# Optimization experiments

Measured on AMD Instinct MI355X. Metric: run time of the kernel, lower is better.

Reference implementation:

```python
import jax, jax.numpy as jnp
import numpy as np

B, L, H = 4, 512, 768          # batch, seq_len, bert hidden
S, R = 100, 100                # num candidate spans, num relation pairs
E = 128                        # size embedding dim
TE, TR = 8, 6                  # entity / relation types
MAX_ENT_LEN = 100
NEG = -1e20


def _span_masks(rng, b, n, seq_len, max_len):
    # contiguous span masks with lengths in [1, max_len-1] so sum(-1) < max_len
    starts = rng.integers(0, seq_len - 1, size=(b, n))
    lengths = rng.integers(1, max_len, size=(b, n))
    ends = np.minimum(starts + lengths, seq_len)
    pos = np.arange(seq_len)
    m = (pos[None, None, :] >= starts[..., None]) & (pos[None, None, :] < ends[..., None])
    return jnp.asarray(m.astype(np.int32))


def setup_inputs() -> dict:
    rng = np.random.default_rng(0)
    key = jax.random.key(0)
    k = jax.random.split(key, 6)
    return {
        "last_hidden_state": jax.random.normal(k[0], (B, L, H), jnp.float32),
        "entity_mask": _span_masks(rng, B, S, L, MAX_ENT_LEN),
        "relations": jnp.asarray(rng.integers(0, S, size=(B, R, 2)).astype(np.int32)),
        "relation_context_mask": _span_masks(rng, B, R, L, MAX_ENT_LEN),
        "relation_sample_mask": jnp.asarray(rng.integers(0, 2, size=(B, R)).astype(np.int32)),
        "size_emb": jax.random.normal(k[1], (MAX_ENT_LEN, E), jnp.float32) * 0.02,
        "span_w": jax.random.normal(k[2], (E + 2 * H, TE), jnp.float32) * 0.02,
        "span_b": jnp.zeros((TE,), jnp.float32),
        "rel_w": jax.random.normal(k[3], (2 * E + 3 * H, TR), jnp.float32) * 0.02,
        "rel_b": jnp.zeros((TR,), jnp.float32),
    }


def _masked_max(h, mask):
    # h: [B,L,H], mask: [B,N,L] int {0,1} -> [B,N,H]
    mf = mask[..., None].astype(h.dtype)                       # [B,N,L,1]
    masked = jnp.where(mf == 0, jnp.asarray(NEG, h.dtype), h[:, None] * mf)
    return masked.max(axis=2)


def reference(last_hidden_state, entity_mask, relations, relation_context_mask,
              relation_sample_mask, size_emb, span_w, span_b, rel_w, rel_b):
    b = last_hidden_state.shape[0]
    # ---- entity classification ----
    context = last_hidden_state[:, 0]                          # CLS pooling [B,H]
    entity_size = size_emb[entity_mask.sum(-1)]                # [B,S,E]
    entity = _masked_max(last_hidden_state, entity_mask)       # [B,S,H]
    ctx = jnp.broadcast_to(context[:, None], (b, entity.shape[1], context.shape[-1]))
    entity_repr = jnp.concatenate([entity, ctx, entity_size], axis=-1)
    entity_logit = entity_repr @ span_w + span_b               # [B,S,TE]
    # ---- relation classification ----
    rel_ctx = _masked_max(last_hidden_state, relation_context_mask)  # [B,R,H]
    rel_ctx = jnp.where(relation_sample_mask[..., None] == 1,
                        jnp.zeros((), rel_ctx.dtype), rel_ctx)
    r = relations.shape[1]
    flat = relations.reshape(b, r * 2)                         # [B,2R]
    pair = jnp.take_along_axis(entity, flat[..., None], axis=1).reshape(b, r, -1)      # [B,R,2H]
    pair_size = jnp.take_along_axis(entity_size, flat[..., None], axis=1).reshape(b, r, -1)  # [B,R,2E]
    relation_repr = jnp.concatenate([rel_ctx, pair, pair_size], axis=-1)
    relation_logit = relation_repr @ rel_w + rel_b             # [B,R,TR]
    return entity_logit, relation_logit
```

## Files before the change

### kernel.cpp

```cpp
#include <hip/hip_runtime.h>

#define Bn 4
#define Ln 512
#define Hn 768
#define Sn 100
#define Rn 100
#define En 128
#define TEn 8
#define TRn 6
#define NEGF (-1e20f)
#define H4 (Hn / 4)
#define E4 (En / 4)

__device__ __forceinline__ float4 fmax4(float4 a, float4 b) {
    return make_float4(fmaxf(a.x, b.x), fmaxf(a.y, b.y),
                       fmaxf(a.z, b.z), fmaxf(a.w, b.w));
}

__global__ void __launch_bounds__(192)
span_kernel(const float* __restrict__ hid,
            const int* __restrict__ ent_mask,
            const int* __restrict__ rel_mask,
            const int* __restrict__ samp_mask,
            const float* __restrict__ size_emb,
            const float* __restrict__ span_w,
            const float* __restrict__ span_b,
            float* __restrict__ entity,
            float* __restrict__ relctx,
            int* __restrict__ entcnt,
            float* __restrict__ out_ent) {
    int blk = blockIdx.x;
    int tid = threadIdx.x;
    int lane = tid & 63;
    int b = blk / (Sn + Rn);
    int idx = blk % (Sn + Rn);
    bool is_rel = idx >= Sn;
    int span = is_rel ? idx - Sn : idx;

    float4* out4 = (float4*)(is_rel ? relctx + ((size_t)b * Rn + span) * Hn
                                    : entity + ((size_t)b * Sn + span) * Hn) + tid;

    bool zero_out = is_rel && (samp_mask[b * Rn + span] == 1);
    if (zero_out) {
        *out4 = make_float4(0.f, 0.f, 0.f, 0.f);
        return;
    }

    const int* mask = is_rel ? rel_mask + ((size_t)b * Rn + span) * Ln
                             : ent_mask + ((size_t)b * Sn + span) * Ln;
    const int4* m4 = (const int4*)(mask + lane * 8);
    int4 ma = m4[0], mb = m4[1];
    int mm[8] = {ma.x, ma.y, ma.z, ma.w, mb.x, mb.y, mb.z, mb.w};
    int cnt = 0, first = 0x7fffffff, last = -1;
    #pragma unroll
    for (int r = 0; r < 8; ++r) {
        if (mm[r] != 0) {
            int row = lane * 8 + r;
            ++cnt;
            first = min(first, row);
            last = max(last, row);
        }
    }
    #pragma unroll
    for (int off = 1; off < 64; off <<= 1) {
        cnt += __shfl_xor(cnt, off, 64);
        first = min(first, __shfl_xor(first, off, 64));
        last = max(last, __shfl_xor(last, off, 64));
    }
    int start = first, end = last + 1;

    const float4* hb4 = (const float4*)(hid + (size_t)b * Ln * Hn) + tid;
    float4 m = make_float4(NEGF, NEGF, NEGF, NEGF);
    int r = start;
    for (; r + 4 <= end; r += 4) {
        float4 v0 = hb4[(size_t)(r + 0) * H4];
        float4 v1 = hb4[(size_t)(r + 1) * H4];
        float4 v2 = hb4[(size_t)(r + 2) * H4];
        float4 v3 = hb4[(size_t)(r + 3) * H4];
        m = fmax4(m, fmax4(fmax4(v0, v1), fmax4(v2, v3)));
    }
    for (; r < end; ++r)
        m = fmax4(m, hb4[(size_t)r * H4]);

    *out4 = m;

    if (is_rel) return;
    if (tid == 0) entcnt[b * Sn + span] = cnt;

    float acc[TEn];
    #pragma unroll
    for (int t = 0; t < TEn; ++t) acc[t] = 0.0f;

    const float* vv = &m.x;
    #pragma unroll
    for (int j = 0; j < 4; ++j) {
        const float4* w4 = (const float4*)(span_w + (size_t)(4 * tid + j) * TEn);
        float4 wa = w4[0], wb = w4[1];
        acc[0] += vv[j] * wa.x; acc[1] += vv[j] * wa.y;
        acc[2] += vv[j] * wa.z; acc[3] += vv[j] * wa.w;
        acc[4] += vv[j] * wb.x; acc[5] += vv[j] * wb.y;
        acc[6] += vv[j] * wb.z; acc[7] += vv[j] * wb.w;
    }
    float4 c = ((const float4*)(hid + (size_t)b * Ln * Hn))[tid];
    const float* cc = &c.x;
    #pragma unroll
    for (int j = 0; j < 4; ++j) {
        const float4* w4 = (const float4*)(span_w + (size_t)(Hn + 4 * tid + j) * TEn);
        float4 wa = w4[0], wb = w4[1];
        acc[0] += cc[j] * wa.x; acc[1] += cc[j] * wa.y;
        acc[2] += cc[j] * wa.z; acc[3] += cc[j] * wa.w;
        acc[4] += cc[j] * wb.x; acc[5] += cc[j] * wb.y;
        acc[6] += cc[j] * wb.z; acc[7] += cc[j] * wb.w;
    }
    if (tid < E4) {
        float4 sv = ((const float4*)(size_emb + (size_t)cnt * En))[tid];
        const float* ss = &sv.x;
        #pragma unroll
        for (int j = 0; j < 4; ++j) {
            const float4* w4 = (const float4*)(span_w + (size_t)(2 * Hn + 4 * tid + j) * TEn);
            float4 wa = w4[0], wb = w4[1];
            acc[0] += ss[j] * wa.x; acc[1] += ss[j] * wa.y;
            acc[2] += ss[j] * wa.z; acc[3] += ss[j] * wa.w;
            acc[4] += ss[j] * wb.x; acc[5] += ss[j] * wb.y;
            acc[6] += ss[j] * wb.z; acc[7] += ss[j] * wb.w;
        }
    }

    #pragma unroll
    for (int t = 0; t < TEn; ++t)
        #pragma unroll
        for (int off = 32; off > 0; off >>= 1)
            acc[t] += __shfl_down(acc[t], off, 64);
    __shared__ float red[3][TEn];
    int wave = tid >> 6;
    if (lane == 0) {
        #pragma unroll
        for (int t = 0; t < TEn; ++t) red[wave][t] = acc[t];
    }
    __syncthreads();
    if (tid < TEn) {
        float s = span_b[tid];
        #pragma unroll
        for (int w = 0; w < 3; ++w) s += red[w][tid];
        out_ent[(size_t)(b * Sn + span) * TEn + tid] = s;
    }
}

__global__ void __launch_bounds__(256)
rel_logit_kernel(const float* __restrict__ entity,
                 const float* __restrict__ relctx,
                 const int* __restrict__ relations,
                 const int* __restrict__ entcnt,
                 const float* __restrict__ size_emb,
                 const float* __restrict__ rel_w,
                 const float* __restrict__ rel_b,
                 float* __restrict__ out_rel) {
    int blk = blockIdx.x;
    int b = blk / Rn;
    int tid = threadIdx.x;
    int a0 = relations[blk * 2 + 0];
    int a1 = relations[blk * 2 + 1];
    const float4* ctx4 = (const float4*)(relctx + (size_t)blk * Hn);
    const float4* e04  = (const float4*)(entity + ((size_t)b * Sn + a0) * Hn);
    const float4* e14  = (const float4*)(entity + ((size_t)b * Sn + a1) * Hn);
    const float4* s04  = (const float4*)(size_emb + (size_t)entcnt[b * Sn + a0] * En);
    const float4* s14  = (const float4*)(size_emb + (size_t)entcnt[b * Sn + a1] * En);

    float acc[TRn];
    #pragma unroll
    for (int t = 0; t < TRn; ++t) acc[t] = 0.0f;

    const int K4 = 3 * H4 + 2 * E4;
    for (int k4 = tid; k4 < K4; k4 += 256) {
        float4 v;
        if (k4 < H4)               v = ctx4[k4];
        else if (k4 < 2 * H4)      v = e04[k4 - H4];
        else if (k4 < 3 * H4)      v = e14[k4 - 2 * H4];
        else if (k4 < 3 * H4 + E4) v = s04[k4 - 3 * H4];
        else                       v = s14[k4 - 3 * H4 - E4];
        int k = k4 * 4;
        const float* vp = &v.x;
        #pragma unroll
        for (int j = 0; j < 4; ++j) {
            const float2* wr = (const float2*)(rel_w + (size_t)(k + j) * TRn);
            float2 w0 = wr[0], w1 = wr[1], w2 = wr[2];
            acc[0] += vp[j] * w0.x; acc[1] += vp[j] * w0.y;
            acc[2] += vp[j] * w1.x; acc[3] += vp[j] * w1.y;
            acc[4] += vp[j] * w2.x; acc[5] += vp[j] * w2.y;
        }
    }

    #pragma unroll
    for (int t = 0; t < TRn; ++t)
        #pragma unroll
        for (int off = 32; off > 0; off >>= 1)
            acc[t] += __shfl_down(acc[t], off, 64);
    __shared__ float red[4][TRn];
    int wave = tid >> 6, lane = tid & 63;
    if (lane == 0) {
        #pragma unroll
        for (int t = 0; t < TRn; ++t) red[wave][t] = acc[t];
    }
    __syncthreads();
    if (tid < TRn) {
        float s = rel_b[tid];
        #pragma unroll
        for (int w = 0; w < 4; ++w) s += red[w][tid];
        out_rel[(size_t)blk * TRn + tid] = s;
    }
}

extern "C" void kernel_launch(void* const* d_in, const int* in_sizes, int n_in,
                              void* d_out, int out_size, void* d_ws, size_t ws_size,
                              hipStream_t stream) {
    const float* hid       = (const float*)d_in[0];
    const int*   ent_mask  = (const int*)d_in[1];
    const int*   relations = (const int*)d_in[2];
    const int*   rel_mask  = (const int*)d_in[3];
    const int*   samp_mask = (const int*)d_in[4];
    const float* size_emb  = (const float*)d_in[5];
    const float* span_w    = (const float*)d_in[6];
    const float* span_b    = (const float*)d_in[7];
    const float* rel_w     = (const float*)d_in[8];
    const float* rel_b     = (const float*)d_in[9];

    float* out = (float*)d_out;
    float* out_ent = out;
    float* out_rel = out + Bn * Sn * TEn;

    char* ws = (char*)d_ws;
    float* entity = (float*)ws;
    float* relctx = entity + (size_t)Bn * Sn * Hn;
    int*   entcnt = (int*)(relctx + (size_t)Bn * Rn * Hn);

    span_kernel<<<Bn * (Sn + Rn), 192, 0, stream>>>(
        hid, ent_mask, rel_mask, samp_mask, size_emb, span_w, span_b,
        entity, relctx, entcnt, out_ent);

    rel_logit_kernel<<<Bn * Rn, 256, 0, stream>>>(
        entity, relctx, relations, entcnt, size_emb, rel_w, rel_b, out_rel);
}
```

Measured before the change: 26.22 us.

## Precompute 8-row block maxima and fuse span max with logits into one kernel

Adds a first kernel that reduces the hidden states into per-8-row block maxima. A single logits kernel then computes span maxima from these block maxima plus partial edge rows. The relation blocks recompute their pair entity maxima directly rather than reading a materialized entity/relctx workspace. This trades redundant recomputation of entity span maxima in relation blocks for removing the large intermediate writes and the dependency between span and relation stages. Span count now uses end-start, which assumes contiguous masks.

```diff
diff --git a/kernel.cpp b/kernel.cpp
--- a/kernel.cpp
+++ b/kernel.cpp
@@ -9,6 +9,8 @@
 #define TEn 8
 #define TRn 6
 #define NEGF (-1e20f)
+#define W 8
+#define NBLK (Ln / W)
 #define H4 (Hn / 4)
 #define E4 (En / 4)
 
@@ -18,195 +20,242 @@
 }
 
 __global__ void __launch_bounds__(192)
-span_kernel(const float* __restrict__ hid,
-            const int* __restrict__ ent_mask,
-            const int* __restrict__ rel_mask,
-            const int* __restrict__ samp_mask,
-            const float* __restrict__ size_emb,
-            const float* __restrict__ span_w,
-            const float* __restrict__ span_b,
-            float* __restrict__ entity,
-            float* __restrict__ relctx,
-            int* __restrict__ entcnt,
-            float* __restrict__ out_ent) {
-    int blk = blockIdx.x;
+blockmax_kernel(const float* __restrict__ hid, float* __restrict__ bmax) {
+    int bj = blockIdx.x;
+    int b = bj / NBLK, j = bj % NBLK;
     int tid = threadIdx.x;
-    int lane = tid & 63;
-    int b = blk / (Sn + Rn);
-    int idx = blk % (Sn + Rn);
-    bool is_rel = idx >= Sn;
-    int span = is_rel ? idx - Sn : idx;
-
-    float4* out4 = (float4*)(is_rel ? relctx + ((size_t)b * Rn + span) * Hn
-                                    : entity + ((size_t)b * Sn + span) * Hn) + tid;
-
-    bool zero_out = is_rel && (samp_mask[b * Rn + span] == 1);
-    if (zero_out) {
-        *out4 = make_float4(0.f, 0.f, 0.f, 0.f);
-        return;
-    }
-
-    const int* mask = is_rel ? rel_mask + ((size_t)b * Rn + span) * Ln
-                             : ent_mask + ((size_t)b * Sn + span) * Ln;
+    const float4* src = (const float4*)(hid + ((size_t)b * Ln + j * W) * Hn);
+    float4 m = src[tid];
+    #pragma unroll
+    for (int r = 1; r < W; ++r)
+        m = fmax4(m, src[(size_t)r * H4 + tid]);
+    ((float4*)(bmax + (size_t)bj * Hn))[tid] = m;
+}
+
+__device__ __forceinline__ void scan_span(const int* __restrict__ mask,
+                                          int lane, int* start, int* end) {
     const int4* m4 = (const int4*)(mask + lane * 8);
-    int4 ma = m4[0], mb = m4[1];
-    int mm[8] = {ma.x, ma.y, ma.z, ma.w, mb.x, mb.y, mb.z, mb.w};
-    int cnt = 0, first = 0x7fffffff, last = -1;
+    int4 a = m4[0], c = m4[1];
+    int mm[8] = {a.x, a.y, a.z, a.w, c.x, c.y, c.z, c.w};
+    int first = 0x7fffffff, last = -1;
     #pragma unroll
     for (int r = 0; r < 8; ++r) {
         if (mm[r] != 0) {
             int row = lane * 8 + r;
-            ++cnt;
             first = min(first, row);
             last = max(last, row);
         }
     }
     #pragma unroll
     for (int off = 1; off < 64; off <<= 1) {
-        cnt += __shfl_xor(cnt, off, 64);
         first = min(first, __shfl_xor(first, off, 64));
         last = max(last, __shfl_xor(last, off, 64));
     }
-    int start = first, end = last + 1;
-
-    const float4* hb4 = (const float4*)(hid + (size_t)b * Ln * Hn) + tid;
+    *start = first;
+    *end = last + 1;
+}
+
+__device__ __forceinline__ float4 span_max(const float4* __restrict__ hb4,
+                                           const float4* __restrict__ bm4,
+                                           int start, int end) {
     float4 m = make_float4(NEGF, NEGF, NEGF, NEGF);
-    int r = start;
-    for (; r + 4 <= end; r += 4) {
-        float4 v0 = hb4[(size_t)(r + 0) * H4];
-        float4 v1 = hb4[(size_t)(r + 1) * H4];
-        float4 v2 = hb4[(size_t)(r + 2) * H4];
-        float4 v3 = hb4[(size_t)(r + 3) * H4];
-        m = fmax4(m, fmax4(fmax4(v0, v1), fmax4(v2, v3)));
-    }
-    for (; r < end; ++r)
+    int jstart = (start + 7) >> 3, jend = end >> 3;
+    if (jstart >= jend) {
+        for (int r = start; r < end; ++r)
+            m = fmax4(m, hb4[(size_t)r * H4]);
+        return m;
+    }
+    int j = jstart;
+    for (; j + 2 <= jend; j += 2)
+        m = fmax4(m, fmax4(bm4[(size_t)j * H4], bm4[(size_t)(j + 1) * H4]));
+    for (; j < jend; ++j)
+        m = fmax4(m, bm4[(size_t)j * H4]);
+    for (int r = start; r < jstart * W; ++r)
         m = fmax4(m, hb4[(size_t)r * H4]);
-
-    *out4 = m;
-
-    if (is_rel) return;
-    if (tid == 0) entcnt[b * Sn + span] = cnt;
-
-    float acc[TEn];
-    #pragma unroll
-    for (int t = 0; t < TEn; ++t) acc[t] = 0.0f;
-
-    const float* vv = &m.x;
-    #pragma unroll
-    for (int j = 0; j < 4; ++j) {
-        const float4* w4 = (const float4*)(span_w + (size_t)(4 * tid + j) * TEn);
-        float4 wa = w4[0], wb = w4[1];
-        acc[0] += vv[j] * wa.x; acc[1] += vv[j] * wa.y;
-        acc[2] += vv[j] * wa.z; acc[3] += vv[j] * wa.w;
-        acc[4] += vv[j] * wb.x; acc[5] += vv[j] * wb.y;
-        acc[6] += vv[j] * wb.z; acc[7] += vv[j] * wb.w;
-    }
-    float4 c = ((const float4*)(hid + (size_t)b * Ln * Hn))[tid];
-    const float* cc = &c.x;
-    #pragma unroll
-    for (int j = 0; j < 4; ++j) {
-        const float4* w4 = (const float4*)(span_w + (size_t)(Hn + 4 * tid + j) * TEn);
-        float4 wa = w4[0], wb = w4[1];
-        acc[0] += cc[j] * wa.x; acc[1] += cc[j] * wa.y;
-        acc[2] += cc[j] * wa.z; acc[3] += cc[j] * wa.w;
-        acc[4] += cc[j] * wb.x; acc[5] += cc[j] * wb.y;
-        acc[6] += cc[j] * wb.z; acc[7] += cc[j] * wb.w;
-    }
-    if (tid < E4) {
-        float4 sv = ((const float4*)(size_emb + (size_t)cnt * En))[tid];
-        const float* ss = &sv.x;
-        #pragma unroll
-        for (int j = 0; j < 4; ++j) {
-            const float4* w4 = (const float4*)(span_w + (size_t)(2 * Hn + 4 * tid + j) * TEn);
-            float4 wa = w4[0], wb = w4[1];
-            acc[0] += ss[j] * wa.x; acc[1] += ss[j] * wa.y;
-            acc[2] += ss[j] * wa.z; acc[3] += ss[j] * wa.w;
-            acc[4] += ss[j] * wb.x; acc[5] += ss[j] * wb.y;
-            acc[6] += ss[j] * wb.z; acc[7] += ss[j] * wb.w;
-        }
-    }
-
-    #pragma unroll
-    for (int t = 0; t < TEn; ++t)
-        #pragma unroll
-        for (int off = 32; off > 0; off >>= 1)
-            acc[t] += __shfl_down(acc[t], off, 64);
-    __shared__ float red[3][TEn];
-    int wave = tid >> 6;
-    if (lane == 0) {
-        #pragma unroll
-        for (int t = 0; t < TEn; ++t) red[wave][t] = acc[t];
-    }
-    __syncthreads();
-    if (tid < TEn) {
-        float s = span_b[tid];
-        #pragma unroll
-        for (int w = 0; w < 3; ++w) s += red[w][tid];
-        out_ent[(size_t)(b * Sn + span) * TEn + tid] = s;
-    }
+    for (int r = jend * W; r < end; ++r)
+        m = fmax4(m, hb4[(size_t)r * H4]);
+    return m;
 }
 
 __global__ void __launch_bounds__(256)
-rel_logit_kernel(const float* __restrict__ entity,
-                 const float* __restrict__ relctx,
-                 const int* __restrict__ relations,
-                 const int* __restrict__ entcnt,
-                 const float* __restrict__ size_emb,
-                 const float* __restrict__ rel_w,
-                 const float* __restrict__ rel_b,
-                 float* __restrict__ out_rel) {
+logits_kernel(const float* __restrict__ hid,
+              const int* __restrict__ ent_mask,
+              const int* __restrict__ rel_mask,
+              const int* __restrict__ samp_mask,
+              const int* __restrict__ relations,
+              const float* __restrict__ size_emb,
+              const float* __restrict__ span_w,
+              const float* __restrict__ span_b,
+              const float* __restrict__ rel_w,
+              const float* __restrict__ rel_b,
+              const float* __restrict__ bmax,
+              float* __restrict__ out_ent,
+              float* __restrict__ out_rel) {
     int blk = blockIdx.x;
-    int b = blk / Rn;
     int tid = threadIdx.x;
-    int a0 = relations[blk * 2 + 0];
-    int a1 = relations[blk * 2 + 1];
-    const float4* ctx4 = (const float4*)(relctx + (size_t)blk * Hn);
-    const float4* e04  = (const float4*)(entity + ((size_t)b * Sn + a0) * Hn);
-    const float4* e14  = (const float4*)(entity + ((size_t)b * Sn + a1) * Hn);
-    const float4* s04  = (const float4*)(size_emb + (size_t)entcnt[b * Sn + a0] * En);
-    const float4* s14  = (const float4*)(size_emb + (size_t)entcnt[b * Sn + a1] * En);
-
-    float acc[TRn];
-    #pragma unroll
-    for (int t = 0; t < TRn; ++t) acc[t] = 0.0f;
-
-    const int K4 = 3 * H4 + 2 * E4;
-    for (int k4 = tid; k4 < K4; k4 += 256) {
-        float4 v;
-        if (k4 < H4)               v = ctx4[k4];
-        else if (k4 < 2 * H4)      v = e04[k4 - H4];
-        else if (k4 < 3 * H4)      v = e14[k4 - 2 * H4];
-        else if (k4 < 3 * H4 + E4) v = s04[k4 - 3 * H4];
-        else                       v = s14[k4 - 3 * H4 - E4];
-        int k = k4 * 4;
-        const float* vp = &v.x;
-        #pragma unroll
-        for (int j = 0; j < 4; ++j) {
-            const float2* wr = (const float2*)(rel_w + (size_t)(k + j) * TRn);
-            float2 w0 = wr[0], w1 = wr[1], w2 = wr[2];
-            acc[0] += vp[j] * w0.x; acc[1] += vp[j] * w0.y;
-            acc[2] += vp[j] * w1.x; acc[3] += vp[j] * w1.y;
-            acc[4] += vp[j] * w2.x; acc[5] += vp[j] * w2.y;
-        }
-    }
-
-    #pragma unroll
-    for (int t = 0; t < TRn; ++t)
-        #pragma unroll
-        for (int off = 32; off > 0; off >>= 1)
-            acc[t] += __shfl_down(acc[t], off, 64);
-    __shared__ float red[4][TRn];
-    int wave = tid >> 6, lane = tid & 63;
-    if (lane == 0) {
-        #pragma unroll
-        for (int t = 0; t < TRn; ++t) red[wave][t] = acc[t];
-    }
-    __syncthreads();
-    if (tid < TRn) {
-        float s = rel_b[tid];
-        #pragma unroll
-        for (int w = 0; w < 4; ++w) s += red[w][tid];
-        out_rel[(size_t)blk * TRn + tid] = s;
+    int lane = tid & 63, wv = tid >> 6;
+
+    __shared__ int se[3][2];
+    __shared__ float red[4][TEn];
+
+    if (blk < Bn * Sn) {
+        int b = blk / Sn;
+        if (wv == 0) {
+            int s0, e0;
+            scan_span(ent_mask + (size_t)blk * Ln, lane, &s0, &e0);
+            if (lane == 0) { se[0][0] = s0; se[0][1] = e0; }
+        }
+        __syncthreads();
+        int start = se[0][0], end = se[0][1];
+        int cnt = end - start;
+
+        float acc[TEn];
+        #pragma unroll
+        for (int t = 0; t < TEn; ++t) acc[t] = 0.0f;
+
+        if (tid < H4) {
+            const float4* hb4 = (const float4*)(hid + (size_t)b * Ln * Hn) + tid;
+            const float4* bm4 = (const float4*)(bmax + (size_t)b * NBLK * Hn) + tid;
+            float4 m = span_max(hb4, bm4, start, end);
+
+            const float* vv = &m.x;
+            #pragma unroll
+            for (int j = 0; j < 4; ++j) {
+                const float4* w4 = (const float4*)(span_w + (size_t)(4 * tid + j) * TEn);
+                float4 wa = w4[0], wb = w4[1];
+                acc[0] += vv[j] * wa.x; acc[1] += vv[j] * wa.y;
+                acc[2] += vv[j] * wa.z; acc[3] += vv[j] * wa.w;
+                acc[4] += vv[j] * wb.x; acc[5] += vv[j] * wb.y;
+                acc[6] += vv[j] * wb.z; acc[7] += vv[j] * wb.w;
+            }
+            float4 c = ((const float4*)(hid + (size_t)b * Ln * Hn))[tid];
+            const float* cc = &c.x;
+            #pragma unroll
+            for (int j = 0; j < 4; ++j) {
+                const float4* w4 = (const float4*)(span_w + (size_t)(Hn + 4 * tid + j) * TEn);
+                float4 wa = w4[0], wb = w4[1];
+                acc[0] += cc[j] * wa.x; acc[1] += cc[j] * wa.y;
+                acc[2] += cc[j] * wa.z; acc[3] += cc[j] * wa.w;
+                acc[4] += cc[j] * wb.x; acc[5] += cc[j] * wb.y;
+                acc[6] += cc[j] * wb.z; acc[7] += cc[j] * wb.w;
+            }
+        } else if (tid >= 192 && tid < 192 + E4) {
+            int u = tid - 192;
+            float4 sv = ((const float4*)(size_emb + (size_t)cnt * En))[u];
+            const float* ss = &sv.x;
+            #pragma unroll
+            for (int j = 0; j < 4; ++j) {
+                const float4* w4 = (const float4*)(span_w + (size_t)(2 * Hn + 4 * u + j) * TEn);
+                float4 wa = w4[0], wb = w4[1];
+                acc[0] += ss[j] * wa.x; acc[1] += ss[j] * wa.y;
+                acc[2] += ss[j] * wa.z; acc[3] += ss[j] * wa.w;
+                acc[4] += ss[j] * wb.x; acc[5] += ss[j] * wb.y;
+                acc[6] += ss[j] * wb.z; acc[7] += ss[j] * wb.w;
+            }
+        }
+
+        #pragma unroll
+        for (int t = 0; t < TEn; ++t)
+            #pragma unroll
+            for (int off = 32; off > 0; off >>= 1)
+                acc[t] += __shfl_down(acc[t], off, 64);
+        if (lane == 0) {
+            #pragma unroll
+            for (int t = 0; t < TEn; ++t) red[wv][t] = acc[t];
+        }
+        __syncthreads();
+        if (tid < TEn) {
+            float s = span_b[tid];
+            #pragma unroll
+            for (int w = 0; w < 4; ++w) s += red[w][tid];
+            out_ent[(size_t)blk * TEn + tid] = s;
+        }
+    } else {
+        int rblk = blk - Bn * Sn;
+        int b = rblk / Rn;
+        int a0 = relations[rblk * 2 + 0];
+        int a1 = relations[rblk * 2 + 1];
+        bool samp = (samp_mask[rblk] == 1);
+
+        if (wv == 0) {
+            int s0, e0;
+            scan_span(ent_mask + ((size_t)b * Sn + a0) * Ln, lane, &s0, &e0);
+            if (lane == 0) { se[0][0] = s0; se[0][1] = e0; }
+        } else if (wv == 1) {
+            int s1, e1;
+            scan_span(ent_mask + ((size_t)b * Sn + a1) * Ln, lane, &s1, &e1);
+            if (lane == 0) { se[1][0] = s1; se[1][1] = e1; }
+        } else if (wv == 2 && !samp) {
+            int s2, e2;
+            scan_span(rel_mask + (size_t)rblk * Ln, lane, &s2, &e2);
+            if (lane == 0) { se[2][0] = s2; se[2][1] = e2; }
+        }
+        __syncthreads();
+        int cnt0 = se[0][1] - se[0][0];
+        int cnt1 = se[1][1] - se[1][0];
+
+        float acc[TRn];
+        #pragma unroll
+        for (int t = 0; t < TRn; ++t) acc[t] = 0.0f;
+
+        if (tid < H4) {
+            const float4* hb4 = (const float4*)(hid + (size_t)b * Ln * Hn) + tid;
+            const float4* bm4 = (const float4*)(bmax + (size_t)b * NBLK * Hn) + tid;
+
+            float4 ve0 = span_max(hb4, bm4, se[0][0], se[0][1]);
+            float4 ve1 = span_max(hb4, bm4, se[1][0], se[1][1]);
+            float4 vc = samp ? make_float4(0.f, 0.f, 0.f, 0.f)
+                             : span_max(hb4, bm4, se[2][0], se[2][1]);
+
+            const float* vp;
+            #pragma unroll
+            for (int seg = 0; seg < 3; ++seg) {
+                float4 v = (seg == 0) ? vc : (seg == 1) ? ve0 : ve1;
+                vp = &v.x;
+                int k4 = seg * H4 + tid;
+                #pragma unroll
+                for (int j = 0; j < 4; ++j) {
+                    const float2* wr = (const float2*)(rel_w + (size_t)(4 * k4 + j) * TRn);
+                    float2 w0 = wr[0], w1 = wr[1], w2 = wr[2];
+                    acc[0] += vp[j] * w0.x; acc[1] += vp[j] * w0.y;
+                    acc[2] += vp[j] * w1.x; acc[3] += vp[j] * w1.y;
+                    acc[4] += vp[j] * w2.x; acc[5] += vp[j] * w2.y;
+                }
+            }
+        } else if (tid >= 192) {
+            int u = tid - 192;
+            int k4, srow;
+            if (u < E4) { srow = cnt0; k4 = 3 * H4 + u; }
+            else        { srow = cnt1; k4 = 3 * H4 + E4 + (u - E4); }
+            int uu = (u < E4) ? u : u - E4;
+            float4 sv = ((const float4*)(size_emb + (size_t)srow * En))[uu];
+            const float* sp = &sv.x;
+            #pragma unroll
+            for (int j = 0; j < 4; ++j) {
+                const float2* wr = (const float2*)(rel_w + (size_t)(4 * k4 + j) * TRn);
+                float2 w0 = wr[0], w1 = wr[1], w2 = wr[2];
+                acc[0] += sp[j] * w0.x; acc[1] += sp[j] * w0.y;
+                acc[2] += sp[j] * w1.x; acc[3] += sp[j] * w1.y;
+                acc[4] += sp[j] * w2.x; acc[5] += sp[j] * w2.y;
+            }
+        }
+
+        #pragma unroll
+        for (int t = 0; t < TRn; ++t)
+            #pragma unroll
+            for (int off = 32; off > 0; off >>= 1)
+                acc[t] += __shfl_down(acc[t], off, 64);
+        if (lane == 0) {
+            #pragma unroll
+            for (int t = 0; t < TRn; ++t) red[wv][t] = acc[t];
+        }
+        __syncthreads();
+        if (tid < TRn) {
+            float s = rel_b[tid];
+            #pragma unroll
+            for (int w = 0; w < 4; ++w) s += red[w][tid];
+            out_rel[(size_t)rblk * TRn + tid] = s;
+        }
     }
 }
 
@@ -228,15 +277,11 @@
     float* out_ent = out;
     float* out_rel = out + Bn * Sn * TEn;
 
-    char* ws = (char*)d_ws;
-    float* entity = (float*)ws;
-    float* relctx = entity + (size_t)Bn * Sn * Hn;
-    int*   entcnt = (int*)(relctx + (size_t)Bn * Rn * Hn);
-
-    span_kernel<<<Bn * (Sn + Rn), 192, 0, stream>>>(
-        hid, ent_mask, rel_mask, samp_mask, size_emb, span_w, span_b,
-        entity, relctx, entcnt, out_ent);
-
-    rel_logit_kernel<<<Bn * Rn, 256, 0, stream>>>(
-        entity, relctx, relations, entcnt, size_emb, rel_w, rel_b, out_rel);
-}
+    float* bmax = (float*)d_ws;
+
+    blockmax_kernel<<<Bn * NBLK, 192, 0, stream>>>(hid, bmax);
+
+    logits_kernel<<<Bn * (Sn + Rn), 256, 0, stream>>>(
+        hid, ent_mask, rel_mask, samp_mask, relations, size_emb,
+        span_w, span_b, rel_w, rel_b, bmax, out_ent, out_rel);
+}
```

Result: faster. 24.62 us (-6.1%).
